# Kernel tuning notes

Hardware: AMD Instinct MI355X
Metric: run time of the kernel (lower is better)

Reference implementation:

```python
import jax, jax.numpy as jnp
import numpy as np

B, S, H, DH, DM = 1024, 32, 32, 32, 1024  # seq==heads==head_dim==32 forced by module's reshapes


def setup_inputs() -> dict:
    key = jax.random.key(0)
    k1, k2 = jax.random.split(key)
    x = jax.random.normal(k1, (B, S, DM), dtype=jnp.float32)
    mask = jnp.ones((1, 1, S, DH), dtype=bool)
    W_qkv = jax.random.normal(k2, (DM, 3 * H * DH), dtype=jnp.float32) / np.sqrt(DM).astype(np.float32)
    return {"x": x, "mask": mask, "W_qkv": W_qkv}


def _rope(t, sin, cos):
    # t: [B, S, H, DH]; sin/cos: [S] broadcast over the HEADS axis (axis 2), as in the original
    t1, t2 = jnp.split(t, 2, axis=-1)
    rot = jnp.concatenate([-t2, t1], axis=-1)
    return t * cos.reshape(1, 1, -1, 1) + rot * sin.reshape(1, 1, -1, 1)


def reference(x, mask, W_qkv):
    b, seq_len, _ = x.shape
    qkv = x @ W_qkv  # [B, S, 3*H*DH]
    q, k, v = jnp.split(qkv, 3, axis=-1)
    q = q.reshape(b, -1, H, DH)
    k = k.reshape(b, -1, H, DH)
    v = v.reshape(b, -1, H, DH)
    pos = jnp.arange(seq_len, dtype=x.dtype)
    sin, cos = jnp.sin(pos), jnp.cos(pos)
    q = _rope(q, sin, cos)
    k = _rope(k, sin, cos)
    # matmul over heads axis (faithful to original): [B,S,H,DH] @ [B,S,DH,H] -> [B,S,H,H]
    attn = jnp.matmul(q, k.transpose(0, 1, 3, 2)) / jnp.sqrt(jnp.asarray(DH, x.dtype))
    attn = attn.reshape(b, H, seq_len, DH)  # valid only because H == 32
    attn = jnp.where(jnp.broadcast_to(mask, attn.shape), attn, -jnp.inf)
    attn = jax.nn.softmax(attn, axis=-1)
    out = jnp.matmul(attn, v)  # [B,H,S,DH] @ [B,S,H,DH]; batched since S==H==32
    return out.reshape(-1, seq_len, H * DH)
```

## Files before the change

kernel.cpp:

```cpp
#include <hip/hip_runtime.h>

typedef __bf16 bf16_t;
typedef __bf16 bf16x4 __attribute__((ext_vector_type(4)));
typedef __bf16 bf16x8 __attribute__((ext_vector_type(8)));
typedef float f32x4 __attribute__((ext_vector_type(4)));
typedef float f32x16 __attribute__((ext_vector_type(16)));
typedef unsigned int uint4v __attribute__((ext_vector_type(4)));

#define M_TOT 32768
#define N_TOT 3072
#define K_TOT 1024

#define WT_BYTES (3072u * 1024u * 2u)
#define XB_BYTES ((size_t)M_TOT * 1024 * 2)

#define SLOT 32768

__device__ __forceinline__ void gload_lds16(const void* g, void* l) {
  __builtin_amdgcn_global_load_lds(
      (const __attribute__((address_space(1))) unsigned int*)g,
      (__attribute__((address_space(3))) unsigned int*)l, 16, 0, 0);
}

__device__ __forceinline__ unsigned pk2(float a, float b) {
  unsigned short lo = __builtin_bit_cast(unsigned short, (bf16_t)a);
  unsigned short hi = __builtin_bit_cast(unsigned short, (bf16_t)b);
  return ((unsigned)hi << 16) | (unsigned)lo;
}

__global__ __launch_bounds__(256) void k_wt(const float* __restrict__ W,
                                            bf16_t* __restrict__ wt) {
  __shared__ float tile[64][65];
  const int c0 = blockIdx.x * 64, k0 = blockIdx.y * 64;
  const int t = threadIdx.x;
  for (int rep = 0; rep < 16; ++rep) {
    int lin = rep * 256 + t;
    int kl = lin >> 6, cl = lin & 63;
    tile[kl][cl] = W[(size_t)(k0 + kl) * 3072 + (c0 + cl)];
  }
  __syncthreads();
  const float scale = 0.17677669529663687f;
  for (int rep = 0; rep < 16; ++rep) {
    int lin = rep * 256 + t;
    int cl = lin >> 6, kl = lin & 63;
    int c = c0 + cl;
    float val;
    if (c < 2048) {
      int cc = c & 1023;
      int h = cc >> 5, d = cc & 31;
      float cv = cosf((float)h), sv = sinf((float)h);
      int clp = cl + ((d < 16) ? 16 : -16);
      float other = tile[kl][clp];
      val = tile[kl][cl] * cv + ((d < 16) ? -other : other) * sv;
      if (c < 1024) val *= scale;
    } else {
      val = tile[kl][cl];
    }
    wt[(size_t)c * 1024 + (k0 + kl)] = (bf16_t)val;
  }
}

__global__ __launch_bounds__(256) void k_xb(const float* __restrict__ x,
                                            bf16_t* __restrict__ xb) {
  const size_t nf4 = (size_t)M_TOT * K_TOT / 4;
  const float4* src = (const float4*)x;
  for (size_t i = (size_t)blockIdx.x * 256 + threadIdx.x; i < nf4;
       i += (size_t)gridDim.x * 256) {
    float4 a = src[i];
    bf16x4 o;
    o[0] = (bf16_t)a.x; o[1] = (bf16_t)a.y; o[2] = (bf16_t)a.z; o[3] = (bf16_t)a.w;
    *(bf16x4*)(&xb[i * 4]) = o;
  }
}

template <int MODE>
__device__ __forceinline__ void ktile(const char* sR, const char* sRn, char* sW,
                                      const char* aT, const char* bT, int w,
                                      int aoffLo, int boffLo,
                                      f32x4 (&acc)[8][4],
                                      bf16x8 (&a)[4], bf16x8 (&b)[4]) {
  bf16x8 a2[4];

  if constexpr (MODE == 0) gload_lds16(aT, sW + w * 1024);
  b[2] = *(const bf16x8*)(sR + (boffLo ^ 64));
  b[3] = *(const bf16x8*)(sR + ((boffLo + 8192) ^ 64));
  asm volatile("s_waitcnt lgkmcnt(2)" ::: "memory");
  __builtin_amdgcn_sched_barrier(0);
  __builtin_amdgcn_s_setprio(1);
#pragma unroll
  for (int m = 0; m < 4; ++m)
#pragma unroll
    for (int n = 0; n < 2; ++n)
      acc[m][n] = __builtin_amdgcn_mfma_f32_16x16x32_bf16(a[m], b[n], acc[m][n], 0, 0, 0);
  __builtin_amdgcn_s_setprio(0);

  if constexpr (MODE == 0) gload_lds16(bT, sW + 16384 + w * 1024);
#pragma unroll
  for (int m = 0; m < 4; ++m)
    a2[m] = *(const bf16x8*)(sR + ((aoffLo + m * 4096) ^ 64));
  asm volatile("s_waitcnt lgkmcnt(4)" ::: "memory");
  __builtin_amdgcn_sched_barrier(0);
  __builtin_amdgcn_s_setprio(1);
#pragma unroll
  for (int m = 0; m < 4; ++m)
#pragma unroll
    for (int n = 2; n < 4; ++n)
      acc[m][n] = __builtin_amdgcn_mfma_f32_16x16x32_bf16(a[m], b[n], acc[m][n], 0, 0, 0);
  __builtin_amdgcn_s_setprio(0);

  if constexpr (MODE == 0) gload_lds16(aT + 64 * 2048, sW + 8192 + w * 1024);
  asm volatile("s_waitcnt lgkmcnt(0)" ::: "memory");
  __builtin_amdgcn_sched_barrier(0);
  __builtin_amdgcn_s_setprio(1);
#pragma unroll
  for (int m = 0; m < 4; ++m)
#pragma unroll
    for (int n = 2; n < 4; ++n)
      acc[m + 4][n] = __builtin_amdgcn_mfma_f32_16x16x32_bf16(a2[m], b[n], acc[m + 4][n], 0, 0, 0);
  __builtin_amdgcn_s_setprio(0);

  if constexpr (MODE == 0) {
    gload_lds16(bT + 64 * 2048, sW + 24576 + w * 1024);
    asm volatile("s_waitcnt vmcnt(4)" ::: "memory");
  } else if constexpr (MODE == 1) {
    asm volatile("s_waitcnt vmcnt(0)" ::: "memory");
  }
  if constexpr (MODE <= 1) {
    __builtin_amdgcn_s_barrier();
    __builtin_amdgcn_sched_barrier(0);
#pragma unroll
    for (int m = 0; m < 4; ++m)
      a[m] = *(const bf16x8*)(sRn + aoffLo + m * 4096);
    __builtin_amdgcn_sched_barrier(0);
  }
  __builtin_amdgcn_s_setprio(1);
#pragma unroll
  for (int m = 0; m < 4; ++m)
#pragma unroll
    for (int n = 0; n < 2; ++n)
      acc[m + 4][n] = __builtin_amdgcn_mfma_f32_16x16x32_bf16(a2[m], b[n], acc[m + 4][n], 0, 0, 0);
  __builtin_amdgcn_s_setprio(0);
  if constexpr (MODE <= 1) {
    b[0] = *(const bf16x8*)(sRn + boffLo);
    b[1] = *(const bf16x8*)(sRn + boffLo + 8192);
  }
}

__global__ __launch_bounds__(512, 2) void k_gemm(const bf16_t* __restrict__ xb,
                                                 const bf16_t* __restrict__ wt,
                                                 bf16_t* __restrict__ qk,
                                                 bf16_t* __restrict__ vb) {
  __shared__ __attribute__((aligned(16))) char lds[3 * SLOT];
  const int tid = threadIdx.x;
  const int w = tid >> 6, lane = tid & 63;
  const int wr = w >> 2, wc = w & 3;

  const int bid = blockIdx.x;
  const int swz = (bid & 7) * 192 + (bid >> 3);
  const int tm = swz / 12, tn = swz % 12;
  const int row0 = tm * 256, col0 = tn * 256;

  const int j = lane >> 3;
  const int u = (lane & 7) ^ j;
  const int half = u >> 2, kk = u & 3;
  const char* aS = (const char*)xb + (size_t)(row0 + half * 128 + w * 8 + j) * 2048 + kk * 16;
  const char* bS = (const char*)wt + (size_t)(col0 + half * 128 + w * 8 + j) * 2048 + kk * 16;

  const int rsel = lane & 15, kslot = lane >> 4;
  const int kswz = ((kslot ^ (rsel & 7)) << 4);
  const int aoffLo = (wr * 16 + rsel) * 128 + kswz;
  const int boffLo = 16384 + (wc * 16 + rsel) * 128 + kswz;

  f32x4 acc[8][4];
#pragma unroll
  for (int m = 0; m < 8; ++m)
#pragma unroll
    for (int n = 0; n < 4; ++n)
#pragma unroll
      for (int i = 0; i < 4; ++i) acc[m][n][i] = 0.f;

  bf16x8 a[4], b[4];

  {
    gload_lds16(aS,                lds + w * 1024);
    gload_lds16(bS,                lds + 16384 + w * 1024);
    gload_lds16(aS + 64 * 2048,    lds + 8192 + w * 1024);
    gload_lds16(bS + 64 * 2048,    lds + 24576 + w * 1024);
    gload_lds16(aS + 64,             lds + SLOT + w * 1024);
    gload_lds16(bS + 64,             lds + SLOT + 16384 + w * 1024);
    gload_lds16(aS + 64 * 2048 + 64, lds + SLOT + 8192 + w * 1024);
    gload_lds16(bS + 64 * 2048 + 64, lds + SLOT + 24576 + w * 1024);
    asm volatile("s_waitcnt vmcnt(4)" ::: "memory");
    __builtin_amdgcn_s_barrier();
    __builtin_amdgcn_sched_barrier(0);
#pragma unroll
    for (int m = 0; m < 4; ++m)
      a[m] = *(const bf16x8*)(lds + aoffLo + m * 4096);
    b[0] = *(const bf16x8*)(lds + boffLo);
    b[1] = *(const bf16x8*)(lds + boffLo + 8192);
  }

  int s0 = 0, s1 = 1, s2 = 2;
  for (int t = 0; t < 30; ++t) {
    ktile<0>(lds + s0 * SLOT, lds + s1 * SLOT, lds + s2 * SLOT,
             aS + (size_t)(t + 2) * 64, bS + (size_t)(t + 2) * 64,
             w, aoffLo, boffLo, acc, a, b);
    const int tmp = s0; s0 = s1; s1 = s2; s2 = tmp;
  }
  ktile<1>(lds + s0 * SLOT, lds + s1 * SLOT, lds, aS, bS, w, aoffLo, boffLo, acc, a, b);
  ktile<2>(lds + s1 * SLOT, lds, lds, aS, bS, w, aoffLo, boffLo, acc, a, b);

  const bool isv = (col0 >= 2048);
  const int rgrp = (lane >> 4) * 4;
#pragma unroll
  for (int m = 0; m < 8; ++m)
#pragma unroll
    for (int n = 0; n < 4; ++n)
#pragma unroll
      for (int reg = 0; reg < 4; ++reg) {
        const int R = row0 + wr * 16 + m * 32 + rgrp + reg;
        const int C = col0 + wc * 16 + n * 64 + rsel;
        const bf16_t val = (bf16_t)acc[m][n][reg];
        if (!isv) qk[(size_t)R * 2048 + C] = val;
        else      vb[(size_t)R * 1024 + (C - 2048)] = val;
      }
}

__global__ __launch_bounds__(256) void k_attn(const bf16_t* __restrict__ qk,
                                              const bf16_t* __restrict__ vb,
                                              float* __restrict__ out) {
  __shared__ __attribute__((aligned(16))) bf16_t vl[4][1024];
  const int t = threadIdx.x;
  const int w = t >> 6, lane = t & 63;
  const int r = blockIdx.x * 4 + w;
  const int jm = lane & 31, hi = lane >> 5;

  const char* vsrc = (const char*)vb + (size_t)r * 2048;
  gload_lds16(vsrc + lane * 16, (char*)vl[w]);
  gload_lds16(vsrc + 1024 + lane * 16, (char*)vl[w] + 1024);

  const char* rowbase = (const char*)qk + (size_t)r * 4096;
  const bf16x8 ak0 = *(const bf16x8*)(rowbase + 2048 + jm * 64 + hi * 16);
  const bf16x8 ak1 = *(const bf16x8*)(rowbase + 2048 + jm * 64 + 32 + hi * 16);
  const bf16x8 bq0 = *(const bf16x8*)(rowbase + jm * 64 + hi * 16);
  const bf16x8 bq1 = *(const bf16x8*)(rowbase + jm * 64 + 32 + hi * 16);

  f32x16 s;
  for (int i = 0; i < 16; ++i) s[i] = 0.f;
  s = __builtin_amdgcn_mfma_f32_32x32x16_bf16(ak0, bq0, s, 0, 0, 0);
  s = __builtin_amdgcn_mfma_f32_32x32x16_bf16(ak1, bq1, s, 0, 0, 0);

  float mx = s[0];
#pragma unroll
  for (int i = 1; i < 16; ++i) mx = fmaxf(mx, s[i]);
  mx = fmaxf(mx, __shfl_xor(mx, 32));
  float p[16];
  float sum = 0.f;
#pragma unroll
  for (int i = 0; i < 16; ++i) { p[i] = __expf(s[i] - mx); sum += p[i]; }
  sum += __shfl_xor(sum, 32);
  const float inv = 1.f / sum;
#pragma unroll
  for (int i = 0; i < 16; ++i) p[i] *= inv;

  const unsigned t01 = pk2(p[0], p[1]),  t23 = pk2(p[2], p[3]);
  const unsigned t45 = pk2(p[4], p[5]),  t67 = pk2(p[6], p[7]);
  const unsigned t89 = pk2(p[8], p[9]),  tab = pk2(p[10], p[11]);
  const unsigned tcd = pk2(p[12], p[13]), tef = pk2(p[14], p[15]);
  const unsigned x01 = (unsigned)__shfl_xor((int)t01, 32), x23 = (unsigned)__shfl_xor((int)t23, 32);
  const unsigned x45 = (unsigned)__shfl_xor((int)t45, 32), x67 = (unsigned)__shfl_xor((int)t67, 32);
  const unsigned x89 = (unsigned)__shfl_xor((int)t89, 32), xab = (unsigned)__shfl_xor((int)tab, 32);
  const unsigned xcd = (unsigned)__shfl_xor((int)tcd, 32), xef = (unsigned)__shfl_xor((int)tef, 32);
  uint4v u0, u1;
  u0[0] = hi ? x45 : t01; u0[1] = hi ? x67 : t23; u0[2] = hi ? t45 : x01; u0[3] = hi ? t67 : x23;
  u1[0] = hi ? xcd : t89; u1[1] = hi ? xef : tab; u1[2] = hi ? tcd : x89; u1[3] = hi ? tef : xab;
  const bf16x8 pa0 = __builtin_bit_cast(bf16x8, u0);
  const bf16x8 pa1 = __builtin_bit_cast(bf16x8, u1);

  asm volatile("s_waitcnt vmcnt(0)" ::: "memory");
  union { bf16x8 v; bf16_t e[8]; } v0, v1;
#pragma unroll
  for (int e = 0; e < 8; ++e) v0.e[e] = vl[w][(8 * hi + e) * 32 + jm];
#pragma unroll
  for (int e = 0; e < 8; ++e) v1.e[e] = vl[w][(16 + 8 * hi + e) * 32 + jm];

  f32x16 o;
  for (int i = 0; i < 16; ++i) o[i] = 0.f;
  o = __builtin_amdgcn_mfma_f32_32x32x16_bf16(pa0, v0.v, o, 0, 0, 0);
  o = __builtin_amdgcn_mfma_f32_32x32x16_bf16(pa1, v1.v, o, 0, 0, 0);

  float* orow = out + (size_t)r * 1024;
#pragma unroll
  for (int reg = 0; reg < 16; ++reg) {
    const int jrow = (reg & 3) + 8 * (reg >> 2) + 4 * hi;
    orow[jrow * 32 + jm] = o[reg];
  }
}

extern "C" void kernel_launch(void* const* d_in, const int* in_sizes, int n_in,
                              void* d_out, int out_size, void* d_ws, size_t ws_size,
                              hipStream_t stream) {
  const float* x = (const float*)d_in[0];
  const float* W = (const float*)d_in[2];

  char* ws = (char*)d_ws;
  bf16_t* wt = (bf16_t*)ws;
  bf16_t* xb = (bf16_t*)(ws + WT_BYTES);
  bf16_t* vb = (bf16_t*)(ws + WT_BYTES + XB_BYTES);

  k_wt <<<dim3(48, 16), 256, 0, stream>>>(W, wt);
  k_xb <<<16384, 256, 0, stream>>>(x, xb);
  k_gemm<<<1536, 512, 0, stream>>>(xb, wt, (bf16_t*)d_out, vb);
  k_attn<<<8192, 256, 0, stream>>>((const bf16_t*)d_out, vb, (float*)d_out);
}
```

Before: 301.5 us.

## Restructure GEMM K-loop: per-wave A/B split loads, 64B rows, unrolled triple buffer

Reworks the bf16 GEMM main loop so each wave loads only A or only B rows, 64-byte-wide LDS rows with a new XOR swizzle, and a statically unrolled three-slot ring instead of rotating slot indices. All fragments for a K-tile are loaded at the start of each tile rather than prefetched across tiles, with staged lgkmcnt waits between MFMA groups. The aim is to simplify addressing and cut register pressure and slot-index overhead. The cost is that the cross-tile LDS-read prefetch is lost, which may expose LDS latency.

```diff
diff --git a/kernel.cpp b/kernel.cpp
--- a/kernel.cpp
+++ b/kernel.cpp
@@ -73,18 +73,30 @@
   }
 }
 
-template <int MODE>
-__device__ __forceinline__ void ktile(const char* sR, const char* sRn, char* sW,
-                                      const char* aT, const char* bT, int w,
-                                      int aoffLo, int boffLo,
-                                      f32x4 (&acc)[8][4],
-                                      bf16x8 (&a)[4], bf16x8 (&b)[4]) {
-  bf16x8 a2[4];
-
-  if constexpr (MODE == 0) gload_lds16(aT, sW + w * 1024);
-  b[2] = *(const bf16x8*)(sR + (boffLo ^ 64));
-  b[3] = *(const bf16x8*)(sR + ((boffLo + 8192) ^ 64));
-  asm volatile("s_waitcnt lgkmcnt(2)" ::: "memory");
+template <int STAGE, int VM>
+__device__ __forceinline__ void ktile(const char* sR, char* sW,
+                                      const char* src, int dstOff,
+                                      int aoff, int boff,
+                                      f32x4 (&acc)[8][4]) {
+  if constexpr (STAGE) {
+#pragma unroll
+    for (int c = 0; c < 4; ++c)
+      gload_lds16(src + c * 32768, sW + dstOff + c * 1024);
+  }
+  bf16x8 a[8], b[4];
+#pragma unroll
+  for (int m = 0; m < 4; ++m) a[m] = *(const bf16x8*)(sR + aoff + m * 2048);
+  b[0] = *(const bf16x8*)(sR + boff);
+  b[1] = *(const bf16x8*)(sR + boff + 4096);
+  __builtin_amdgcn_sched_barrier(0);
+  b[2] = *(const bf16x8*)(sR + boff + 8192);
+  b[3] = *(const bf16x8*)(sR + boff + 12288);
+  __builtin_amdgcn_sched_barrier(0);
+#pragma unroll
+  for (int m = 4; m < 8; ++m) a[m] = *(const bf16x8*)(sR + aoff + m * 2048);
+  __builtin_amdgcn_sched_barrier(0);
+
+  asm volatile("s_waitcnt lgkmcnt(6)" ::: "memory");
   __builtin_amdgcn_sched_barrier(0);
   __builtin_amdgcn_s_setprio(1);
 #pragma unroll
@@ -94,56 +106,34 @@
       acc[m][n] = __builtin_amdgcn_mfma_f32_16x16x32_bf16(a[m], b[n], acc[m][n], 0, 0, 0);
   __builtin_amdgcn_s_setprio(0);
 
-  if constexpr (MODE == 0) gload_lds16(bT, sW + 16384 + w * 1024);
+  asm volatile("s_waitcnt lgkmcnt(4)" ::: "memory");
+  __builtin_amdgcn_sched_barrier(0);
+  __builtin_amdgcn_s_setprio(1);
 #pragma unroll
   for (int m = 0; m < 4; ++m)
-    a2[m] = *(const bf16x8*)(sR + ((aoffLo + m * 4096) ^ 64));
-  asm volatile("s_waitcnt lgkmcnt(4)" ::: "memory");
+#pragma unroll
+    for (int n = 2; n < 4; ++n)
+      acc[m][n] = __builtin_amdgcn_mfma_f32_16x16x32_bf16(a[m], b[n], acc[m][n], 0, 0, 0);
+  __builtin_amdgcn_s_setprio(0);
+
+  asm volatile("s_waitcnt lgkmcnt(0)" ::: "memory");
   __builtin_amdgcn_sched_barrier(0);
   __builtin_amdgcn_s_setprio(1);
 #pragma unroll
-  for (int m = 0; m < 4; ++m)
+  for (int m = 4; m < 8; ++m)
 #pragma unroll
     for (int n = 2; n < 4; ++n)
       acc[m][n] = __builtin_amdgcn_mfma_f32_16x16x32_bf16(a[m], b[n], acc[m][n], 0, 0, 0);
+#pragma unroll
+  for (int m = 4; m < 8; ++m)
+#pragma unroll
+    for (int n = 0; n < 2; ++n)
+      acc[m][n] = __builtin_amdgcn_mfma_f32_16x16x32_bf16(a[m], b[n], acc[m][n], 0, 0, 0);
   __builtin_amdgcn_s_setprio(0);
 
-  if constexpr (MODE == 0) gload_lds16(aT + 64 * 2048, sW + 8192 + w * 1024);
-  asm volatile("s_waitcnt lgkmcnt(0)" ::: "memory");
-  __builtin_amdgcn_sched_barrier(0);
-  __builtin_amdgcn_s_setprio(1);
-#pragma unroll
-  for (int m = 0; m < 4; ++m)
-#pragma unroll
-    for (int n = 2; n < 4; ++n)
-      acc[m + 4][n] = __builtin_amdgcn_mfma_f32_16x16x32_bf16(a2[m], b[n], acc[m + 4][n], 0, 0, 0);
-  __builtin_amdgcn_s_setprio(0);
-
-  if constexpr (MODE == 0) {
-    gload_lds16(bT + 64 * 2048, sW + 24576 + w * 1024);
-    asm volatile("s_waitcnt vmcnt(4)" ::: "memory");
-  } else if constexpr (MODE == 1) {
-    asm volatile("s_waitcnt vmcnt(0)" ::: "memory");
-  }
-  if constexpr (MODE <= 1) {
-    __builtin_amdgcn_s_barrier();
-    __builtin_amdgcn_sched_barrier(0);
-#pragma unroll
-    for (int m = 0; m < 4; ++m)
-      a[m] = *(const bf16x8*)(sRn + aoffLo + m * 4096);
-    __builtin_amdgcn_sched_barrier(0);
-  }
-  __builtin_amdgcn_s_setprio(1);
-#pragma unroll
-  for (int m = 0; m < 4; ++m)
-#pragma unroll
-    for (int n = 0; n < 2; ++n)
-      acc[m + 4][n] = __builtin_amdgcn_mfma_f32_16x16x32_bf16(a2[m], b[n], acc[m + 4][n], 0, 0, 0);
-  __builtin_amdgcn_s_setprio(0);
-  if constexpr (MODE <= 1) {
-    b[0] = *(const bf16x8*)(sRn + boffLo);
-    b[1] = *(const bf16x8*)(sRn + boffLo + 8192);
-  }
+  if constexpr (VM == 4) asm volatile("s_waitcnt vmcnt(4)" ::: "memory");
+  else if constexpr (VM == 0) asm volatile("s_waitcnt vmcnt(0)" ::: "memory");
+  if constexpr (VM >= 0) __builtin_amdgcn_s_barrier();
 }
 
 __global__ __launch_bounds__(512, 2) void k_gemm(const bf16_t* __restrict__ xb,
@@ -160,16 +150,18 @@
   const int tm = swz / 12, tn = swz % 12;
   const int row0 = tm * 256, col0 = tn * 256;
 
-  const int j = lane >> 3;
-  const int u = (lane & 7) ^ j;
-  const int half = u >> 2, kk = u & 3;
-  const char* aS = (const char*)xb + (size_t)(row0 + half * 128 + w * 8 + j) * 2048 + kk * 16;
-  const char* bS = (const char*)wt + (size_t)(col0 + half * 128 + w * 8 + j) * 2048 + kk * 16;
-
-  const int rsel = lane & 15, kslot = lane >> 4;
-  const int kswz = ((kslot ^ (rsel & 7)) << 4);
-  const int aoffLo = (wr * 16 + rsel) * 128 + kswz;
-  const int boffLo = 16384 + (wc * 16 + rsel) * 128 + kswz;
+  const int isB = w >> 2;
+  const int rL = (w & 3) * 64 + (lane >> 2);
+  const int g = (lane & 3) ^ ((lane >> 3) & 3);
+  const char* src = isB
+      ? (const char*)wt + (size_t)(col0 + rL) * 2048 + g * 16
+      : (const char*)xb + (size_t)(row0 + rL) * 2048 + g * 16;
+  const int dstOff = (w & 3) * 4096 + isB * 16384;
+
+  const int rsel = lane & 15;
+  const int kx = (((lane >> 4) ^ ((rsel >> 1) & 3)) << 4);
+  const int aoff = (wr * 16 + rsel) * 64 + kx;
+  const int boff = 16384 + (wc * 16 + rsel) * 64 + kx;
 
   f32x4 acc[8][4];
 #pragma unroll
@@ -179,36 +171,24 @@
 #pragma unroll
       for (int i = 0; i < 4; ++i) acc[m][n][i] = 0.f;
 
-  bf16x8 a[4], b[4];
-
   {
-    gload_lds16(aS,                lds + w * 1024);
-    gload_lds16(bS,                lds + 16384 + w * 1024);
-    gload_lds16(aS + 64 * 2048,    lds + 8192 + w * 1024);
-    gload_lds16(bS + 64 * 2048,    lds + 24576 + w * 1024);
-    gload_lds16(aS + 64,             lds + SLOT + w * 1024);
-    gload_lds16(bS + 64,             lds + SLOT + 16384 + w * 1024);
-    gload_lds16(aS + 64 * 2048 + 64, lds + SLOT + 8192 + w * 1024);
-    gload_lds16(bS + 64 * 2048 + 64, lds + SLOT + 24576 + w * 1024);
+#pragma unroll
+    for (int c = 0; c < 4; ++c) gload_lds16(src + c * 32768, lds + dstOff + c * 1024);
+#pragma unroll
+    for (int c = 0; c < 4; ++c) gload_lds16(src + 64 + c * 32768, lds + SLOT + dstOff + c * 1024);
     asm volatile("s_waitcnt vmcnt(4)" ::: "memory");
     __builtin_amdgcn_s_barrier();
-    __builtin_amdgcn_sched_barrier(0);
-#pragma unroll
-    for (int m = 0; m < 4; ++m)
-      a[m] = *(const bf16x8*)(lds + aoffLo + m * 4096);
-    b[0] = *(const bf16x8*)(lds + boffLo);
-    b[1] = *(const bf16x8*)(lds + boffLo + 8192);
-  }
-
-  int s0 = 0, s1 = 1, s2 = 2;
-  for (int t = 0; t < 30; ++t) {
-    ktile<0>(lds + s0 * SLOT, lds + s1 * SLOT, lds + s2 * SLOT,
-             aS + (size_t)(t + 2) * 64, bS + (size_t)(t + 2) * 64,
-             w, aoffLo, boffLo, acc, a, b);
-    const int tmp = s0; s0 = s1; s1 = s2; s2 = tmp;
-  }
-  ktile<1>(lds + s0 * SLOT, lds + s1 * SLOT, lds, aS, bS, w, aoffLo, boffLo, acc, a, b);
-  ktile<2>(lds + s1 * SLOT, lds, lds, aS, bS, w, aoffLo, boffLo, acc, a, b);
+  }
+
+  const char* p = src + 128;
+  for (int i = 0; i < 10; ++i) {
+    ktile<1, 4>(lds,            lds + 2 * SLOT, p,       dstOff, aoff, boff, acc);
+    ktile<1, 4>(lds + SLOT,     lds,            p + 64,  dstOff, aoff, boff, acc);
+    ktile<1, 4>(lds + 2 * SLOT, lds + SLOT,     p + 128, dstOff, aoff, boff, acc);
+    p += 192;
+  }
+  ktile<0, 0>(lds, lds, src, dstOff, aoff, boff, acc);
+  ktile<0, -1>(lds + SLOT, lds, src, dstOff, aoff, boff, acc);
 
   const bool isv = (col0 >= 2048);
   const int rgrp = (lane >> 4) * 4;
```

Result: no change. 305.9 us (+1.5%).
